# Kernel tuning notes

Hardware: AMD Instinct MI355X
Metric: run time of the kernel (lower is better)

The kernel has to match this reference:

```python
import jax, jax.numpy as jnp
import numpy as np

EPS = 1e-5
NUM_HEADS = 8
POOL_K = 50
POOL_S = 15
DEPTH = 4


def _conv2d(x, w, b, pad_h, pad_w):
    y = jax.lax.conv_general_dilated(
        x, w, window_strides=(1, 1),
        padding=((pad_h, pad_h), (pad_w, pad_w)),
        dimension_numbers=('NCHW', 'OIHW', 'NCHW'))
    return y + b[None, :, None, None]


def _bn_eval(x, g, b):
    # eval-mode BatchNorm2d with running_mean=0, running_var=1
    s = g / jnp.sqrt(1.0 + EPS)
    return x * s[None, :, None, None] + b[None, :, None, None]


def _layernorm(x, g, b):
    m = x.mean(-1, keepdims=True)
    v = ((x - m) ** 2).mean(-1, keepdims=True)
    return (x - m) / jnp.sqrt(v + EPS) * g + b


def _mha(x, wq, bq, wk, bk, wv, bv, wo, bo):
    B, n, d = x.shape
    def split(h):
        return h.reshape(B, n, NUM_HEADS, -1).transpose(0, 2, 1, 3)  # b h n dk
    q = split(x @ wq.T + bq)
    k = split(x @ wk.T + bk)
    v = split(x @ wv.T + bv)
    dk = q.shape[-1]
    scores = jnp.einsum('bhqd,bhkd->bhqk', q, k) / jnp.sqrt(jnp.float32(dk))
    attn = jax.nn.softmax(scores, axis=-1)
    o = jnp.einsum('bhqk,bhkd->bhqd', attn, v).transpose(0, 2, 1, 3).reshape(B, n, d)
    return o @ wo.T + bo


def _encoder(x, p):
    (g1, b1, g2, b2, wq, bq, wk, bk, wv, bv, wo, bo, f1w, f1b, f2w, f2b) = p
    h = _layernorm(x, g1, b1)
    x = x + _mha(h, wq, bq, wk, bk, wv, bv, wo, bo)
    h = _layernorm(x, g2, b2)
    ff = jax.nn.gelu(h @ f1w.T + f1b, approximate=False) @ f2w.T + f2b
    return x + ff


def _forward(x, tw1, tb1, tw2, tb2, tw3, tb3, tw4, tb4, bn1_g, bn1_b, sw, sb,
             bn2_g, bn2_b, ln1_g, ln1_b, ln2_g, ln2_b, wq, bq, wk, bk, wv, bv,
             wo, bo, f1w, f1b, f2w, f2b, ew, eb, bn3_g, bn3_b, cw, cb):
    B, C, T = x.shape
    xi = x[:, None]  # [B,1,C,T]
    h = jnp.concatenate([
        _conv2d(xi, tw1, tb1, 0, 7),
        _conv2d(xi, tw2, tb2, 0, 12),
        _conv2d(xi, tw3, tb3, 0, 25),
        _conv2d(xi, tw4, tb4, 0, 32)], axis=1)          # [B,D,C,T]
    h = _bn_eval(h, bn1_g, bn1_b)
    h = _conv2d(h, sw, sb, 0, 0)                         # [B,D,1,T]
    h = jax.nn.elu(_bn_eval(h, bn2_g, bn2_b))[:, :, 0]   # [B,D,T]

    npos = (T - POOL_K) // POOL_S + 1
    idx = np.arange(npos)[:, None] * POOL_S + np.arange(POOL_K)  # [n,K]
    win = h[:, :, idx]                                   # [B,D,n,K]
    avg = win.mean(-1)                                   # [B,D,n]
    var = win.var(-1, ddof=1)                            # unbiased, like torch
    vlog = jnp.log(jnp.clip(var, 1e-6, 1e6))
    x1 = avg.transpose(0, 2, 1)                          # [B,n,D]
    x2 = vlog.transpose(0, 2, 1)

    for i in range(DEPTH):
        p = (ln1_g[i], ln1_b[i], ln2_g[i], ln2_b[i], wq[i], bq[i], wk[i], bk[i],
             wv[i], bv[i], wo[i], bo[i], f1w[i], f1b[i], f2w[i], f2b[i])
        x1 = _encoder(x1, p)
        x2 = _encoder(x2, p)

    h = jnp.concatenate([x1[:, :, None, :], x2[:, :, None, :]], axis=2)  # [B,n,2,D]
    h = jax.nn.elu(_bn_eval(_conv2d(h, ew, eb, 0, 0), bn3_g, bn3_b))     # [B,n,1,D]
    return h.reshape(B, -1) @ cw.T + cb


def setup_inputs() -> dict:
    B, C, T, D, n, ff, ncls = 16, 64, 1000, 128, 64, 512, 4
    ks = iter(jax.random.split(jax.random.key(0), 48))
    def nrm(shape, s=0.02):
        return jax.random.normal(next(ks), shape, jnp.float32) * s
    inp = {
        'x': jax.random.normal(next(ks), (B, C, T), jnp.float32),
        'tw1': nrm((D // 4, 1, 1, 15)), 'tb1': jnp.zeros(D // 4),
        'tw2': nrm((D // 4, 1, 1, 25)), 'tb2': jnp.zeros(D // 4),
        'tw3': nrm((D // 4, 1, 1, 51)), 'tb3': jnp.zeros(D // 4),
        'tw4': nrm((D // 4, 1, 1, 65)), 'tb4': jnp.zeros(D // 4),
        'bn1_g': jnp.ones(D), 'bn1_b': jnp.zeros(D),
        'sw': nrm((D, D, C, 1)), 'sb': jnp.zeros(D),
        'bn2_g': jnp.ones(D), 'bn2_b': jnp.zeros(D),
        'ln1_g': jnp.ones((DEPTH, D)), 'ln1_b': jnp.zeros((DEPTH, D)),
        'ln2_g': jnp.ones((DEPTH, D)), 'ln2_b': jnp.zeros((DEPTH, D)),
        'wq': nrm((DEPTH, D, D)), 'bq': jnp.zeros((DEPTH, D)),
        'wk': nrm((DEPTH, D, D)), 'bk': jnp.zeros((DEPTH, D)),
        'wv': nrm((DEPTH, D, D)), 'bv': jnp.zeros((DEPTH, D)),
        'wo': nrm((DEPTH, D, D)), 'bo': jnp.zeros((DEPTH, D)),
        'f1w': nrm((DEPTH, ff, D)), 'f1b': jnp.zeros((DEPTH, ff)),
        'f2w': nrm((DEPTH, D, ff)), 'f2b': jnp.zeros((DEPTH, D)),
        'ew': nrm((n, n, 2, 1)), 'eb': jnp.zeros(n),
        'bn3_g': jnp.ones(n), 'bn3_b': jnp.zeros(n),
        'cw': nrm((ncls, D * n)), 'cb': jnp.zeros(ncls),
    }
    return inp


def reference(x, tw1, tb1, tw2, tb2, tw3, tb3, tw4, tb4, bn1_g, bn1_b, sw, sb,
              bn2_g, bn2_b, ln1_g, ln1_b, ln2_g, ln2_b, wq, bq, wk, bk, wv, bv,
              wo, bo, f1w, f1b, f2w, f2b, ew, eb, bn3_g, bn3_b, cw, cb):
    return _forward(x, tw1, tb1, tw2, tb2, tw3, tb3, tw4, tb4, bn1_g, bn1_b,
                    sw, sb, bn2_g, bn2_b, ln1_g, ln1_b, ln2_g, ln2_b, wq, bq,
                    wk, bk, wv, bv, wo, bo, f1w, f1b, f2w, f2b, ew, eb,
                    bn3_g, bn3_b, cw, cb)
```

## Files before the change

### kernel.cpp

```cpp
#include <hip/hip_runtime.h>
#include <math.h>

typedef unsigned short u16;
typedef __attribute__((ext_vector_type(8))) short frag8;
typedef __attribute__((ext_vector_type(4))) float f32x4;

__device__ __forceinline__ float eluf(float v) { return v > 0.f ? v : expm1f(v); }
__device__ __forceinline__ float geluf(float v) {
  return 0.5f * v * (1.f + erff(v * 0.70710678118654752f));
}
__device__ __forceinline__ u16 f2bf(float f) {
  union { float f; unsigned int i; } v; v.f = f;
  return (u16)((v.i + 0x7fffu + ((v.i >> 16) & 1u)) >> 16);
}

#define BN_S 0.99999500003749969f

__global__ void k_tws1(const float* tw1, const float* tw2, const float* tw3, const float* tw4,
                       const float* tb1, const float* tb2, const float* tb3, const float* tb4,
                       const float* bn1g, const float* bn1b,
                       float* tws1, float* c1) {
  int idx = blockIdx.x * 256 + threadIdx.x;
  if (idx < 8320) {
    int i = idx / 65, u = idx - i * 65;
    int g = i >> 5, il = i & 31;
    const float* tws[4] = {tw1, tw2, tw3, tw4};
    const int P[4] = {7, 12, 25, 32};
    int c = u - 32;
    float s1 = bn1g[i] * BN_S;
    float val = 0.f;
    int p = P[g];
    if (c >= -p && c <= p) val = s1 * tws[g][il * (2 * p + 1) + (c + p)];
    tws1[idx] = val;
  } else if (idx < 8448) {
    int i = idx - 8320;
    int g = i >> 5, il = i & 31;
    const float* tbs[4] = {tb1, tb2, tb3, tb4};
    float s1 = bn1g[i] * BN_S;
    c1[i] = s1 * tbs[g][il] + bn1b[i];
  }
}

__global__ __launch_bounds__(256) void k_weff(const float* __restrict__ sw, const float* __restrict__ sb,
                                              const float* __restrict__ tws1, const float* __restrict__ c1,
                                              u16* __restrict__ Wb, float* __restrict__ biasEff) {
  __shared__ float swl[8192];
  __shared__ float tl[8320];
  const int tid = threadIdx.x, lane = tid & 63, wave = tid >> 6;
  const int o = blockIdx.x;
  for (int idx = tid; idx < 8192; idx += 256) swl[idx] = sw[o * 8192 + idx];
  for (int idx = tid; idx < 8320; idx += 256) tl[idx] = tws1[idx];
  __syncthreads();

  #pragma unroll 1
  for (int j = 0; j < 4; j++) {
    int u0 = (wave + 4 * j) * 4;
    float a[4][4];
    #pragma unroll
    for (int uu = 0; uu < 4; uu++)
      #pragma unroll
      for (int r = 0; r < 4; r++) a[uu][r] = 0.f;
    #pragma unroll 1
    for (int i = 0; i < 128; i += 4) {
      #pragma unroll
      for (int ii = 0; ii < 4; ii++) {
        float s = swl[(i + ii) * 64 + lane];
        #pragma unroll
        for (int uu = 0; uu < 4; uu++)
          a[uu][ii] = fmaf(s, tl[(i + ii) * 65 + u0 + uu], a[uu][ii]);
      }
    }
    #pragma unroll
    for (int uu = 0; uu < 4; uu++)
      Wb[((u0 + uu) * 128 + o) * 64 + lane] = f2bf((a[uu][0] + a[uu][1]) + (a[uu][2] + a[uu][3]));
  }

  if (wave == 0) {
    float a[4] = {0.f, 0.f, 0.f, 0.f};
    #pragma unroll 1
    for (int i = 0; i < 128; i += 4) {
      #pragma unroll
      for (int ii = 0; ii < 4; ii++)
        a[ii] = fmaf(swl[(i + ii) * 64 + lane], tl[(i + ii) * 65 + 64], a[ii]);
    }
    Wb[(64 * 128 + o) * 64 + lane] = f2bf((a[0] + a[1]) + (a[2] + a[3]));
  } else if (wave == 1) {
    float pa = 0.f;
    #pragma unroll 8
    for (int i = 0; i < 128; i++)
      pa = fmaf(swl[i * 64 + lane], c1[i], pa);
    #pragma unroll
    for (int off = 32; off; off >>= 1) pa += __shfl_xor(pa, off);
    if (lane == 0) biasEff[o] = pa + sb[o];
  }
}

__global__ __launch_bounds__(256) void k_conv(const float* __restrict__ x,
                                              const u16* __restrict__ Wb,
                                              const float* __restrict__ biasEff,
                                              const float* __restrict__ bn2g, const float* __restrict__ bn2b,
                                              float* __restrict__ z) {
  __shared__ u16 xs[128 * 88];
  const int tid = threadIdx.x;
  const int t0 = blockIdx.x * 64;
  const int o0 = blockIdx.y * 32;
  const int b  = blockIdx.z;

  #pragma unroll
  for (int i = 0; i < 8; i++) {
    int pos = tid + i * 256;
    int kh = pos >> 5;
    int tt = (pos & 31) * 4;
    int gt = t0 - 32 + tt;
    const float* xp = x + (b * 64 + kh) * 1000;
    float v[4];
    if (gt >= 0 && gt + 3 < 1000) {
      float4 f = *(const float4*)(xp + gt);
      v[0] = f.x; v[1] = f.y; v[2] = f.z; v[3] = f.w;
    } else {
      #pragma unroll
      for (int e = 0; e < 4; e++) { int g2 = gt + e; v[e] = (g2 >= 0 && g2 < 1000) ? xp[g2] : 0.f; }
    }
    #pragma unroll
    for (int e = 0; e < 4; e++) xs[(tt + e) * 88 + kh] = f2bf(v[e]);
  }
  __syncthreads();

  const int lane = tid & 63, wave = tid >> 6;
  const int wt = (wave & 1) * 32;
  const int wo = (wave >> 1) * 16;
  const int m = lane & 15, q = lane >> 4;

  f32x4 acc[2];
  #pragma unroll
  for (int i = 0; i < 2; i++) acc[i] = (f32x4){0.f, 0.f, 0.f, 0.f};

  #pragma unroll 2
  for (int u = 0; u < 65; u++) {
    frag8 A[2][2], B[2];
    #pragma unroll
    for (int tp = 0; tp < 2; tp++)
      #pragma unroll
      for (int kc = 0; kc < 2; kc++)
        A[tp][kc] = *(const frag8*)&xs[(wt + tp * 16 + m + u) * 88 + kc * 32 + q * 8];
    #pragma unroll
    for (int kc = 0; kc < 2; kc++)
      B[kc] = *(const frag8*)(Wb + ((u * 128) + o0 + wo + m) * 64 + kc * 32 + q * 8);
    #pragma unroll
    for (int tp = 0; tp < 2; tp++) {
      acc[tp] = __builtin_amdgcn_mfma_f32_16x16x32_bf16(A[tp][0], B[0], acc[tp], 0, 0, 0);
      acc[tp] = __builtin_amdgcn_mfma_f32_16x16x32_bf16(A[tp][1], B[1], acc[tp], 0, 0, 0);
    }
  }

  {
    int o = o0 + wo + m;
    float s2 = bn2g[o] * BN_S;
    float be = biasEff[o], b2 = bn2b[o];
    #pragma unroll
    for (int tp = 0; tp < 2; tp++) {
      #pragma unroll
      for (int r = 0; r < 4; r++) {
        int t = t0 + wt + tp * 16 + q * 4 + r;
        if (t < 1000)
          z[(b * 128 + o) * 1000 + t] = eluf((acc[tp][r] + be) * s2 + b2);
      }
    }
  }
}

__global__ __launch_bounds__(256) void k_pool(const float* __restrict__ z, float* __restrict__ X) {
  __shared__ float zl[16 * 1001];
  int b = blockIdx.x, og = blockIdx.y;
  int tid = threadIdx.x;
  const float* zb = z + (b * 128 + og * 16) * 1000;
  #pragma unroll 1
  for (int r = 0; r < 16; r++)
    for (int c = tid; c < 1000; c += 256) zl[r * 1001 + c] = zb[r * 1000 + c];
  __syncthreads();

  int ol = tid & 15;
  int pb = tid >> 4;
  #pragma unroll 1
  for (int pass = 0; pass < 4; pass++) {
    int p = pb + pass * 16;
    const float* zp = zl + ol * 1001 + p * 15;
    float s = 0.f, ss = 0.f;
    #pragma unroll
    for (int k = 0; k < 50; k++) { float v = zp[k]; s += v; ss = fmaf(v, v, ss); }
    float m = s * 0.02f;
    float var = (ss - s * m) * (1.f / 49.f);
    var = fminf(fmaxf(var, 1e-6f), 1e6f);
    int o = og * 16 + ol;
    X[(b * 64 + p) * 128 + o] = m;
    X[((16 + b) * 64 + p) * 128 + o] = logf(var);
  }
}

__global__ __launch_bounds__(256) void k_cvt6(const float* __restrict__ wq, const float* __restrict__ wk,
                                              const float* __restrict__ wv, const float* __restrict__ wo,
                                              const float* __restrict__ f1w, const float* __restrict__ f2w,
                                              u16* __restrict__ out) {
  int i = blockIdx.x * 256 + threadIdx.x;
  if (i >= 196608) return;
  int fi = i * 4;
  const float* src; int off;
  if      (fi < 65536)  { src = wq;  off = fi; }
  else if (fi < 131072) { src = wk;  off = fi - 65536; }
  else if (fi < 196608) { src = wv;  off = fi - 131072; }
  else if (fi < 262144) { src = wo;  off = fi - 196608; }
  else if (fi < 524288) { src = f1w; off = fi - 262144; }
  else                  { src = f2w; off = fi - 524288; }
  float4 v = *(const float4*)(src + off);
  ushort4 p;
  p.x = f2bf(v.x); p.y = f2bf(v.y); p.z = f2bf(v.z); p.w = f2bf(v.w);
  *(ushort4*)(out + fi) = p;
}

__device__ __forceinline__ void ln128(const float* __restrict__ Xs, u16* __restrict__ Hs,
                                      const float* __restrict__ g, const float* __restrict__ b,
                                      int lane, int wave) {
  float g0 = g[lane], g1 = g[64 + lane], b0 = b[lane], b1 = b[64 + lane];
  #pragma unroll
  for (int rr = 0; rr < 8; rr++) {
    int r = wave * 8 + rr;
    float v0 = Xs[r * 132 + lane], v1 = Xs[r * 132 + 64 + lane];
    float s_ = v0 + v1;
    #pragma unroll
    for (int off = 32; off; off >>= 1) s_ += __shfl_xor(s_, off);
    float mn = s_ * (1.f / 128.f);
    float d0 = v0 - mn, d1 = v1 - mn;
    float qq = d0 * d0 + d1 * d1;
    #pragma unroll
    for (int off = 32; off; off >>= 1) qq += __shfl_xor(qq, off);
    float rs = rsqrtf(qq * (1.f / 128.f) + 1e-5f);
    Hs[r * 136 + lane]      = f2bf(d0 * rs * g0 + b0);
    Hs[r * 136 + 64 + lane] = f2bf(d1 * rs * g1 + b1);
  }
}

__device__ __forceinline__ void gemm_hoist(const frag8 Ar[4][4], const frag8 Bf[4], f32x4 acc[4]) {
  #pragma unroll
  for (int kc = 0; kc < 4; kc++)
    #pragma unroll
    for (int mt = 0; mt < 4; mt++)
      acc[mt] = __builtin_amdgcn_mfma_f32_16x16x32_bf16(Ar[mt][kc], Bf[kc], acc[mt], 0, 0, 0);
}

__device__ __forceinline__ void gemm_pref(const u16* __restrict__ Asrc, int astride,
                                          const frag8 Bf[4], int m, int q, f32x4 acc[4]) {
  #pragma unroll
  for (int kc = 0; kc < 4; kc++) {
    #pragma unroll
    for (int mt = 0; mt < 4; mt++) {
      frag8 Af = *(const frag8*)(Asrc + (mt * 16 + m) * astride + kc * 32 + q * 8);
      acc[mt] = __builtin_amdgcn_mfma_f32_16x16x32_bf16(Af, Bf[kc], acc[mt], 0, 0, 0);
    }
  }
}

__global__ __launch_bounds__(512, 1) void k_enc(float* __restrict__ X,
                                                const u16* __restrict__ Wenc,
                                                const float* __restrict__ ln1g, const float* __restrict__ ln1b,
                                                const float* __restrict__ ln2g, const float* __restrict__ ln2b,
                                                const float* __restrict__ bq, const float* __restrict__ bk,
                                                const float* __restrict__ bv, const float* __restrict__ bo,
                                                const float* __restrict__ f1b, const float* __restrict__ f2b) {
  __shared__ __align__(16) float Xs[64 * 132];
  __shared__ __align__(16) u16   Hs[64 * 136];
  __shared__ __align__(16) u16   Qb[8 * 64 * 32];
  __shared__ __align__(16) u16   Kb[8 * 64 * 32];
  __shared__ __align__(16) u16   VtAO[8 * 16 * 80 + 64 * 136];
  u16* Vt   = VtAO;
  u16* AOs  = VtAO + 10240;
  u16* F1a  = VtAO;
  u16* F1b_ = VtAO + 8704;

  const int tid = threadIdx.x;
  const int lane = tid & 63, wave = tid >> 6;
  const int m = lane & 15, q = lane >> 4;
  const int n0 = wave * 16;
  float* Xg = X + blockIdx.x * 64 * 128;

  const u16* WQ  = Wenc;
  const u16* WK  = Wenc + 65536;
  const u16* WV  = Wenc + 131072;
  const u16* WO  = Wenc + 196608;
  const u16* F1W = Wenc + 262144;
  const u16* F2W = Wenc + 524288;

  u16* Qh = Qb + wave * 2048;
  u16* Kh = Kb + wave * 2048;
  u16* Vh = Vt + wave * 1280;

  for (int i = tid; i < 8192; i += 512) Xs[(i >> 7) * 132 + (i & 127)] = Xg[i];
  __syncthreads();

  #pragma unroll 1
  for (int l = 0; l < 4; l++) {
    const u16* wqb  = WQ  + l * 16384;
    const u16* wkb  = WK  + l * 16384;
    const u16* wvb  = WV  + l * 16384;
    const u16* wob  = WO  + l * 16384;
    const u16* f1wb = F1W + l * 65536;
    const u16* f2wb = F2W + l * 65536;

    frag8 fq[4], fk[4], fv[4];
    #pragma unroll
    for (int kc = 0; kc < 4; kc++) {
      fq[kc] = *(const frag8*)(wqb + (n0 + m) * 128 + kc * 32 + q * 8);
      fk[kc] = *(const frag8*)(wkb + (n0 + m) * 128 + kc * 32 + q * 8);
      fv[kc] = *(const frag8*)(wvb + (n0 + m) * 128 + kc * 32 + q * 8);
    }

    ln128(Xs, Hs, ln1g + l * 128, ln1b + l * 128, lane, wave);
    __syncthreads();

    frag8 fo[4];
    #pragma unroll
    for (int kc = 0; kc < 4; kc++)
      fo[kc] = *(const frag8*)(wob + (n0 + m) * 128 + kc * 32 + q * 8);
    {
      frag8 Ar[4][4];
      #pragma unroll
      for (int mt = 0; mt < 4; mt++)
        #pragma unroll
        for (int kc = 0; kc < 4; kc++)
          Ar[mt][kc] = *(const frag8*)&Hs[(mt * 16 + m) * 136 + kc * 32 + q * 8];
      f32x4 aq[4], ak[4], av[4];
      #pragma unroll
      for (int mt = 0; mt < 4; mt++) { aq[mt] = (f32x4){0,0,0,0}; ak[mt] = (f32x4){0,0,0,0}; av[mt] = (f32x4){0,0,0,0}; }
      gemm_hoist(Ar, fq, aq);
      gemm_hoist(Ar, fk, ak);
      gemm_hoist(Ar, fv, av);
      float bqv = bq[l * 128 + n0 + m];
      float bkv = bk[l * 128 + n0 + m];
      float bvv = bv[l * 128 + n0 + m];
      #pragma unroll
      for (int mt = 0; mt < 4; mt++)
        #pragma unroll
        for (int r = 0; r < 4; r++) {
          int row = mt * 16 + q * 4 + r;
          Qh[row * 32 + m] = f2bf((aq[mt][r] + bqv) * 0.25f);
          Kh[row * 32 + m] = f2bf(ak[mt][r] + bkv);
          Vh[m * 80 + row] = f2bf(av[mt][r] + bvv);
        }
      frag8 z8 = {};
      *(frag8*)&Qh[lane * 32 + 16] = z8;
      *(frag8*)&Qh[lane * 32 + 24] = z8;
      *(frag8*)&Kh[lane * 32 + 16] = z8;
      *(frag8*)&Kh[lane * 32 + 24] = z8;
    }

    frag8 f1f[4];
    #pragma unroll
    for (int kc = 0; kc < 4; kc++)
      f1f[kc] = *(const frag8*)(f1wb + (n0 + m) * 128 + kc * 32 + q * 8);
    {
      f32x4 sacc[4][4];
      frag8 QA[4], KB[4];
      #pragma unroll
      for (int mt = 0; mt < 4; mt++) QA[mt] = *(const frag8*)&Qh[(mt * 16 + m) * 32 + q * 8];
      #pragma unroll
      for (int np = 0; np < 4; np++) KB[np] = *(const frag8*)&Kh[(np * 16 + m) * 32 + q * 8];
      #pragma unroll
      for (int mt = 0; mt < 4; mt++)
        #pragma unroll
        for (int np = 0; np < 4; np++)
          sacc[mt][np] = __builtin_amdgcn_mfma_f32_16x16x32_bf16(QA[mt], KB[np], (f32x4){0,0,0,0}, 0, 0, 0);

      float inv[4][4];
      #pragma unroll
      for (int mt = 0; mt < 4; mt++)
        #pragma unroll
        for (int r = 0; r < 4; r++) {
          float mx = fmaxf(fmaxf(sacc[mt][0][r], sacc[mt][1][r]), fmaxf(sacc[mt][2][r], sacc[mt][3][r]));
          #pragma unroll
          for (int off = 1; off < 16; off <<= 1) mx = fmaxf(mx, __shfl_xor(mx, off));
          #pragma unroll
          for (int np = 0; np < 4; np++) sacc[mt][np][r] = __expf(sacc[mt][np][r] - mx);
          float s_ = ((sacc[mt][0][r] + sacc[mt][1][r]) + (sacc[mt][2][r] + sacc[mt][3][r]));
          #pragma unroll
          for (int off = 1; off < 16; off <<= 1) s_ += __shfl_xor(s_, off);
          inv[mt][r] = 1.f / s_;
        }

      #pragma unroll
      for (int mt = 0; mt < 4; mt++)
        #pragma unroll
        for (int np = 0; np < 4; np++) {
          u16* dst = (np < 2) ? Qh : Kh;
          int col = (np & 1) * 16 + m;
          #pragma unroll
          for (int r = 0; r < 4; r++)
            dst[(mt * 16 + q * 4 + r) * 32 + col] = f2bf(sacc[mt][np][r] * inv[mt][r]);
        }

      f32x4 oacc[4];
      #pragma unroll
      for (int mt = 0; mt < 4; mt++) oacc[mt] = (f32x4){0,0,0,0};
      #pragma unroll
      for (int kc = 0; kc < 2; kc++) {
        frag8 VB = *(const frag8*)&Vh[m * 80 + kc * 32 + q * 8];
        const u16* Psrc = kc ? Kh : Qh;
        #pragma unroll
        for (int mt = 0; mt < 4; mt++) {
          frag8 PA = *(const frag8*)&Psrc[(mt * 16 + m) * 32 + q * 8];
          oacc[mt] = __builtin_amdgcn_mfma_f32_16x16x32_bf16(PA, VB, oacc[mt], 0, 0, 0);
        }
      }
      #pragma unroll
      for (int mt = 0; mt < 4; mt++)
        #pragma unroll
        for (int r = 0; r < 4; r++)
          AOs[(mt * 16 + q * 4 + r) * 136 + wave * 16 + m] = f2bf(oacc[mt][r]);
    }
    __syncthreads();

    {
      f32x4 ao4[4];
      #pragma unroll
      for (int mt = 0; mt < 4; mt++) ao4[mt] = (f32x4){0,0,0,0};
      gemm_pref(AOs, 136, fo, m, q, ao4);
      float bov = bo[l * 128 + n0 + m];
      #pragma unroll
      for (int mt = 0; mt < 4; mt++)
        #pragma unroll
        for (int r = 0; r < 4; r++)
          Xs[(mt * 16 + q * 4 + r) * 132 + n0 + m] += ao4[mt][r] + bov;
    }
    __syncthreads();

    ln128(Xs, Hs, ln2g + l * 128, ln2b + l * 128, lane, wave);
    __syncthreads();

    {
      frag8 Ar[4][4];
      #pragma unroll
      for (int mt = 0; mt < 4; mt++)
        #pragma unroll
        for (int kc = 0; kc < 4; kc++)
          Ar[mt][kc] = *(const frag8*)&Hs[(mt * 16 + m) * 136 + kc * 32 + q * 8];
      f32x4 acc2[4];
      #pragma unroll
      for (int mt = 0; mt < 4; mt++) acc2[mt] = (f32x4){0,0,0,0};
      #pragma unroll 1
      for (int c = 0; c < 4; c++) {
        frag8 f2f[4];
        #pragma unroll
        for (int kc = 0; kc < 4; kc++)
          f2f[kc] = *(const frag8*)(f2wb + (n0 + m) * 512 + c * 128 + kc * 32 + q * 8);
        u16* F1c = (c & 1) ? F1b_ : F1a;
        {
          f32x4 a1[4];
          #pragma unroll
          for (int mt = 0; mt < 4; mt++) a1[mt] = (f32x4){0,0,0,0};
          gemm_hoist(Ar, f1f, a1);
          float b1v = f1b[l * 512 + c * 128 + n0 + m];
          #pragma unroll
          for (int mt = 0; mt < 4; mt++)
            #pragma unroll
            for (int r = 0; r < 4; r++)
              F1c[(mt * 16 + q * 4 + r) * 136 + n0 + m] = f2bf(geluf(a1[mt][r] + b1v));
        }
        __syncthreads();
        if (c < 3) {
          #pragma unroll
          for (int kc = 0; kc < 4; kc++)
            f1f[kc] = *(const frag8*)(f1wb + ((c + 1) * 128 + n0 + m) * 128 + kc * 32 + q * 8);
        }
        gemm_pref(F1c, 136, f2f, m, q, acc2);
      }
      float b2v = f2b[l * 128 + n0 + m];
      #pragma unroll
      for (int mt = 0; mt < 4; mt++)
        #pragma unroll
        for (int r = 0; r < 4; r++)
          Xs[(mt * 16 + q * 4 + r) * 132 + n0 + m] += acc2[mt][r] + b2v;
    }
    __syncthreads();
  }

  for (int i = tid; i < 8192; i += 512) Xg[i] = Xs[(i >> 7) * 132 + (i & 127)];
}

__global__ __launch_bounds__(256) void k_head1(const float* __restrict__ X, const float* __restrict__ ew,
                                               const float* __restrict__ eb, const float* __restrict__ g3,
                                               const float* __restrict__ b3, float* __restrict__ G) {
  __shared__ float Xs[2][8192];
  int b = blockIdx.x, ot = blockIdx.y;
  int tid = threadIdx.x;
  {
    const float4* x1 = (const float4*)(X + b * 8192);
    const float4* x2 = (const float4*)(X + (16 + b) * 8192);
    float4* s1 = (float4*)&Xs[0][0];
    float4* s2 = (float4*)&Xs[1][0];
    for (int i = tid; i < 2048; i += 256) { s1[i] = x1[i]; s2[i] = x2[i]; }
  }
  __syncthreads();
  int w = tid & 127, og = tid >> 7;
  int oc0 = ot * 16 + og * 8;
  float a[8] = {};
  for (int ic = 0; ic < 64; ic++) {
    float x1v = Xs[0][ic * 128 + w], x2v = Xs[1][ic * 128 + w];
    #pragma unroll
    for (int j = 0; j < 8; j++) {
      a[j] = fmaf(ew[((oc0 + j) * 64 + ic) * 2 + 0], x1v, a[j]);
      a[j] = fmaf(ew[((oc0 + j) * 64 + ic) * 2 + 1], x2v, a[j]);
    }
  }
  #pragma unroll
  for (int j = 0; j < 8; j++) {
    int oc = oc0 + j;
    float v = (a[j] + eb[oc]) * (g3[oc] * BN_S) + b3[oc];
    G[(b * 64 + oc) * 128 + w] = eluf(v);
  }
}

__global__ __launch_bounds__(256) void k_head2(const float* __restrict__ G, const float* __restrict__ cw,
                                               const float* __restrict__ cb, float* __restrict__ out) {
  __shared__ float red[256];
  int b = blockIdx.x, c = blockIdx.y, tid = threadIdx.x;
  const float4* g4 = (const float4*)(G + b * 8192);
  const float4* c4 = (const float4*)(cw + c * 8192);
  float p = 0.f;
  for (int i = tid; i < 2048; i += 256) {
    float4 g = g4[i], w = c4[i];
    p += g.x * w.x + g.y * w.y + g.z * w.z + g.w * w.w;
  }
  red[tid] = p;
  __syncthreads();
  for (int s = 128; s > 0; s >>= 1) {
    if (tid < s) red[tid] += red[tid + s];
    __syncthreads();
  }
  if (tid == 0) out[b * 4 + c] = red[0] + cb[c];
}

extern "C" void kernel_launch(void* const* d_in, const int* in_sizes, int n_in,
                              void* d_out, int out_size, void* d_ws, size_t ws_size,
                              hipStream_t stream) {
  const float* x    = (const float*)d_in[0];
  const float* tw1  = (const float*)d_in[1];  const float* tb1 = (const float*)d_in[2];
  const float* tw2  = (const float*)d_in[3];  const float* tb2 = (const float*)d_in[4];
  const float* tw3  = (const float*)d_in[5];  const float* tb3 = (const float*)d_in[6];
  const float* tw4  = (const float*)d_in[7];  const float* tb4 = (const float*)d_in[8];
  const float* bn1g = (const float*)d_in[9];  const float* bn1b = (const float*)d_in[10];
  const float* sw   = (const float*)d_in[11]; const float* sb   = (const float*)d_in[12];
  const float* bn2g = (const float*)d_in[13]; const float* bn2b = (const float*)d_in[14];
  const float* ln1g = (const float*)d_in[15]; const float* ln1b = (const float*)d_in[16];
  const float* ln2g = (const float*)d_in[17]; const float* ln2b = (const float*)d_in[18];
  const float* wq   = (const float*)d_in[19]; const float* bq   = (const float*)d_in[20];
  const float* wk   = (const float*)d_in[21]; const float* bk   = (const float*)d_in[22];
  const float* wv   = (const float*)d_in[23]; const float* bv   = (const float*)d_in[24];
  const float* wo   = (const float*)d_in[25]; const float* bo   = (const float*)d_in[26];
  const float* f1w  = (const float*)d_in[27]; const float* f1b  = (const float*)d_in[28];
  const float* f2w  = (const float*)d_in[29]; const float* f2b  = (const float*)d_in[30];
  const float* ew   = (const float*)d_in[31]; const float* eb   = (const float*)d_in[32];
  const float* g3   = (const float*)d_in[33]; const float* b3   = (const float*)d_in[34];
  const float* cw   = (const float*)d_in[35]; const float* cb   = (const float*)d_in[36];

  float* ws      = (float*)d_ws;
  float* tws1    = ws;
  float* c1      = ws + 8320;
  float* biasEff = ws + 8448;
  u16*   Wb      = (u16*)(ws + 8576);
  float* z       = ws + 541056;
  float* X       = ws + 2589056;
  u16*   Wenc    = (u16*)(ws + 3113344);
  float* G       = z;

  k_cvt6<<<768, 256, 0, stream>>>(wq, wk, wv, wo, f1w, f2w, Wenc);
  k_tws1<<<33, 256, 0, stream>>>(tw1, tw2, tw3, tw4, tb1, tb2, tb3, tb4, bn1g, bn1b, tws1, c1);
  k_weff<<<128, 256, 0, stream>>>(sw, sb, tws1, c1, Wb, biasEff);
  k_conv<<<dim3(16, 4, 16), 256, 0, stream>>>(x, Wb, biasEff, bn2g, bn2b, z);
  k_pool<<<dim3(16, 8), 256, 0, stream>>>(z, X);

  k_enc<<<32, 512, 0, stream>>>(X, Wenc, ln1g, ln1b, ln2g, ln2b, bq, bk, bv, bo, f1b, f2b);

  k_head1<<<dim3(16, 4), 256, 0, stream>>>(X, ew, eb, g3, b3, G);
  k_head2<<<dim3(16, 4), 256, 0, stream>>>(G, cw, cb, (float*)d_out);
}
```

Measured before the change: 384.2 us.

## Fuse prep kernels and head kernels, widen conv tile, restructure encoder FFN buffering

Merges the weight-conversion and temporal-weight prep kernels into k_weff, and merges the two head kernels into one per-batch kernel that keeps G in shared memory. This cuts the launch count from eight to five. The conv kernel now computes 64 output channels per block with a register-prefetched B fragment, so each LDS-staged x tile is reused more. The encoder FFN writes all four GELU chunks into a shared pool before running the second GEMM with prefetched weights, which removes the per-chunk barriers. The cost is fewer conv blocks and lower parallelism in the head and conv grids, plus higher LDS use in the encoder.

Result: slower. 403.0 us (+4.9%).

```diff
diff --git a/kernel.cpp b/kernel.cpp
--- a/kernel.cpp
+++ b/kernel.cpp
@@ -16,40 +16,59 @@
 
 #define BN_S 0.99999500003749969f
 
-__global__ void k_tws1(const float* tw1, const float* tw2, const float* tw3, const float* tw4,
-                       const float* tb1, const float* tb2, const float* tb3, const float* tb4,
-                       const float* bn1g, const float* bn1b,
-                       float* tws1, float* c1) {
-  int idx = blockIdx.x * 256 + threadIdx.x;
-  if (idx < 8320) {
-    int i = idx / 65, u = idx - i * 65;
-    int g = i >> 5, il = i & 31;
-    const float* tws[4] = {tw1, tw2, tw3, tw4};
-    const int P[4] = {7, 12, 25, 32};
-    int c = u - 32;
-    float s1 = bn1g[i] * BN_S;
-    float val = 0.f;
-    int p = P[g];
-    if (c >= -p && c <= p) val = s1 * tws[g][il * (2 * p + 1) + (c + p)];
-    tws1[idx] = val;
-  } else if (idx < 8448) {
-    int i = idx - 8320;
-    int g = i >> 5, il = i & 31;
-    const float* tbs[4] = {tb1, tb2, tb3, tb4};
-    float s1 = bn1g[i] * BN_S;
-    c1[i] = s1 * tbs[g][il] + bn1b[i];
-  }
-}
-
-__global__ __launch_bounds__(256) void k_weff(const float* __restrict__ sw, const float* __restrict__ sb,
-                                              const float* __restrict__ tws1, const float* __restrict__ c1,
-                                              u16* __restrict__ Wb, float* __restrict__ biasEff) {
+__global__ __launch_bounds__(256) void k_weff(const float* __restrict__ tw1, const float* __restrict__ tw2,
+                                              const float* __restrict__ tw3, const float* __restrict__ tw4,
+                                              const float* __restrict__ tb1, const float* __restrict__ tb2,
+                                              const float* __restrict__ tb3, const float* __restrict__ tb4,
+                                              const float* __restrict__ bn1g, const float* __restrict__ bn1b,
+                                              const float* __restrict__ sw, const float* __restrict__ sb,
+                                              const float* __restrict__ wq, const float* __restrict__ wk,
+                                              const float* __restrict__ wv, const float* __restrict__ wo,
+                                              const float* __restrict__ f1w, const float* __restrict__ f2w,
+                                              u16* __restrict__ Wb, float* __restrict__ biasEff,
+                                              u16* __restrict__ Wenc) {
   __shared__ float swl[8192];
   __shared__ float tl[8320];
+  __shared__ float c1l[128];
   const int tid = threadIdx.x, lane = tid & 63, wave = tid >> 6;
   const int o = blockIdx.x;
+
   for (int idx = tid; idx < 8192; idx += 256) swl[idx] = sw[o * 8192 + idx];
-  for (int idx = tid; idx < 8320; idx += 256) tl[idx] = tws1[idx];
+  {
+    const float* tws4[4] = {tw1, tw2, tw3, tw4};
+    const int P[4] = {7, 12, 25, 32};
+    for (int idx = tid; idx < 8320; idx += 256) {
+      int i = idx / 65, u = idx - i * 65;
+      int g = i >> 5, il = i & 31;
+      int c = u - 32;
+      float s1 = bn1g[i] * BN_S;
+      float val = 0.f;
+      int p = P[g];
+      if (c >= -p && c <= p) val = s1 * tws4[g][il * (2 * p + 1) + (c + p)];
+      tl[idx] = val;
+    }
+    const float* tbs[4] = {tb1, tb2, tb3, tb4};
+    for (int i = tid; i < 128; i += 256) {
+      int g = i >> 5, il = i & 31;
+      float s1 = bn1g[i] * BN_S;
+      c1l[i] = s1 * tbs[g][il] + bn1b[i];
+    }
+  }
+
+  for (int i = blockIdx.x * 256 + tid; i < 196608; i += 128 * 256) {
+    int fi = i * 4;
+    const float* src; int off;
+    if      (fi < 65536)  { src = wq;  off = fi; }
+    else if (fi < 131072) { src = wk;  off = fi - 65536; }
+    else if (fi < 196608) { src = wv;  off = fi - 131072; }
+    else if (fi < 262144) { src = wo;  off = fi - 196608; }
+    else if (fi < 524288) { src = f1w; off = fi - 262144; }
+    else                  { src = f2w; off = fi - 524288; }
+    float4 v = *(const float4*)(src + off);
+    ushort4 p;
+    p.x = f2bf(v.x); p.y = f2bf(v.y); p.z = f2bf(v.z); p.w = f2bf(v.w);
+    *(ushort4*)(Wenc + fi) = p;
+  }
   __syncthreads();
 
   #pragma unroll 1
@@ -88,7 +107,7 @@
     float pa = 0.f;
     #pragma unroll 8
     for (int i = 0; i < 128; i++)
-      pa = fmaf(swl[i * 64 + lane], c1[i], pa);
+      pa = fmaf(swl[i * 64 + lane], c1l[i], pa);
     #pragma unroll
     for (int off = 32; off; off >>= 1) pa += __shfl_xor(pa, off);
     if (lane == 0) biasEff[o] = pa + sb[o];
@@ -103,7 +122,7 @@
   __shared__ u16 xs[128 * 88];
   const int tid = threadIdx.x;
   const int t0 = blockIdx.x * 64;
-  const int o0 = blockIdx.y * 32;
+  const int o0 = blockIdx.y * 64;
   const int b  = blockIdx.z;
 
   #pragma unroll
@@ -128,33 +147,54 @@
 
   const int lane = tid & 63, wave = tid >> 6;
   const int wt = (wave & 1) * 32;
-  const int wo = (wave >> 1) * 16;
+  const int wo = (wave >> 1) * 32;
   const int m = lane & 15, q = lane >> 4;
 
-  f32x4 acc[2];
+  f32x4 acc[2][2];
   #pragma unroll
-  for (int i = 0; i < 2; i++) acc[i] = (f32x4){0.f, 0.f, 0.f, 0.f};
-
-  #pragma unroll 2
+  for (int i = 0; i < 2; i++)
+    #pragma unroll
+    for (int j = 0; j < 2; j++) acc[i][j] = (f32x4){0.f, 0.f, 0.f, 0.f};
+
+  frag8 Bc[2][2];
+  #pragma unroll
+  for (int op = 0; op < 2; op++)
+    #pragma unroll
+    for (int kc = 0; kc < 2; kc++)
+      Bc[op][kc] = *(const frag8*)(Wb + (o0 + wo + op * 16 + m) * 64 + kc * 32 + q * 8);
+
+  #pragma unroll 1
   for (int u = 0; u < 65; u++) {
-    frag8 A[2][2], B[2];
+    frag8 Bn[2][2];
+    int un = (u < 64) ? u + 1 : 64;
+    #pragma unroll
+    for (int op = 0; op < 2; op++)
+      #pragma unroll
+      for (int kc = 0; kc < 2; kc++)
+        Bn[op][kc] = *(const frag8*)(Wb + ((un * 128) + o0 + wo + op * 16 + m) * 64 + kc * 32 + q * 8);
+    frag8 A[2][2];
     #pragma unroll
     for (int tp = 0; tp < 2; tp++)
       #pragma unroll
       for (int kc = 0; kc < 2; kc++)
         A[tp][kc] = *(const frag8*)&xs[(wt + tp * 16 + m + u) * 88 + kc * 32 + q * 8];
     #pragma unroll
-    for (int kc = 0; kc < 2; kc++)
-      B[kc] = *(const frag8*)(Wb + ((u * 128) + o0 + wo + m) * 64 + kc * 32 + q * 8);
-    #pragma unroll
-    for (int tp = 0; tp < 2; tp++) {
-      acc[tp] = __builtin_amdgcn_mfma_f32_16x16x32_bf16(A[tp][0], B[0], acc[tp], 0, 0, 0);
-      acc[tp] = __builtin_amdgcn_mfma_f32_16x16x32_bf16(A[tp][1], B[1], acc[tp], 0, 0, 0);
-    }
-  }
-
-  {
-    int o = o0 + wo + m;
+    for (int tp = 0; tp < 2; tp++)
+      #pragma unroll
+      for (int op = 0; op < 2; op++) {
+        acc[tp][op] = __builtin_amdgcn_mfma_f32_16x16x32_bf16(A[tp][0], Bc[op][0], acc[tp][op], 0, 0, 0);
+        acc[tp][op] = __builtin_amdgcn_mfma_f32_16x16x32_bf16(A[tp][1], Bc[op][1], acc[tp][op], 0, 0, 0);
+      }
+    #pragma unroll
+    for (int op = 0; op < 2; op++)
+      #pragma unroll
+      for (int kc = 0; kc < 2; kc++)
+        Bc[op][kc] = Bn[op][kc];
+  }
+
+  #pragma unroll
+  for (int op = 0; op < 2; op++) {
+    int o = o0 + wo + op * 16 + m;
     float s2 = bn2g[o] * BN_S;
     float be = biasEff[o], b2 = bn2b[o];
     #pragma unroll
@@ -163,7 +203,7 @@
       for (int r = 0; r < 4; r++) {
         int t = t0 + wt + tp * 16 + q * 4 + r;
         if (t < 1000)
-          z[(b * 128 + o) * 1000 + t] = eluf((acc[tp][r] + be) * s2 + b2);
+          z[(b * 128 + o) * 1000 + t] = eluf((acc[tp][op][r] + be) * s2 + b2);
       }
     }
   }
@@ -197,26 +237,6 @@
   }
 }
 
-__global__ __launch_bounds__(256) void k_cvt6(const float* __restrict__ wq, const float* __restrict__ wk,
-                                              const float* __restrict__ wv, const float* __restrict__ wo,
-                                              const float* __restrict__ f1w, const float* __restrict__ f2w,
-                                              u16* __restrict__ out) {
-  int i = blockIdx.x * 256 + threadIdx.x;
-  if (i >= 196608) return;
-  int fi = i * 4;
-  const float* src; int off;
-  if      (fi < 65536)  { src = wq;  off = fi; }
-  else if (fi < 131072) { src = wk;  off = fi - 65536; }
-  else if (fi < 196608) { src = wv;  off = fi - 131072; }
-  else if (fi < 262144) { src = wo;  off = fi - 196608; }
-  else if (fi < 524288) { src = f1w; off = fi - 262144; }
-  else                  { src = f2w; off = fi - 524288; }
-  float4 v = *(const float4*)(src + off);
-  ushort4 p;
-  p.x = f2bf(v.x); p.y = f2bf(v.y); p.z = f2bf(v.z); p.w = f2bf(v.w);
-  *(ushort4*)(out + fi) = p;
-}
-
 __device__ __forceinline__ void ln128(const float* __restrict__ Xs, u16* __restrict__ Hs,
                                       const float* __restrict__ g, const float* __restrict__ b,
                                       int lane, int wave) {
@@ -268,13 +288,8 @@
                                                 const float* __restrict__ f1b, const float* __restrict__ f2b) {
   __shared__ __align__(16) float Xs[64 * 132];
   __shared__ __align__(16) u16   Hs[64 * 136];
-  __shared__ __align__(16) u16   Qb[8 * 64 * 32];
-  __shared__ __align__(16) u16   Kb[8 * 64 * 32];
-  __shared__ __align__(16) u16   VtAO[8 * 16 * 80 + 64 * 136];
-  u16* Vt   = VtAO;
-  u16* AOs  = VtAO + 10240;
-  u16* F1a  = VtAO;
-  u16* F1b_ = VtAO + 8704;
+  __shared__ __align__(16) u16   Pool[43008];
+  u16* AOs = Hs;
 
   const int tid = threadIdx.x;
   const int lane = tid & 63, wave = tid >> 6;
@@ -289,9 +304,9 @@
   const u16* F1W = Wenc + 262144;
   const u16* F2W = Wenc + 524288;
 
-  u16* Qh = Qb + wave * 2048;
-  u16* Kh = Kb + wave * 2048;
-  u16* Vh = Vt + wave * 1280;
+  u16* Qh = Pool + wave * 2048;
+  u16* Kh = Pool + 16384 + wave * 2048;
+  u16* Vh = Pool + 32768 + wave * 1280;
 
   for (int i = tid; i < 8192; i += 512) Xs[(i >> 7) * 132 + (i & 127)] = Xg[i];
   __syncthreads();
@@ -441,35 +456,49 @@
         #pragma unroll
         for (int kc = 0; kc < 4; kc++)
           Ar[mt][kc] = *(const frag8*)&Hs[(mt * 16 + m) * 136 + kc * 32 + q * 8];
-      f32x4 acc2[4];
-      #pragma unroll
-      for (int mt = 0; mt < 4; mt++) acc2[mt] = (f32x4){0,0,0,0};
       #pragma unroll 1
       for (int c = 0; c < 4; c++) {
-        frag8 f2f[4];
-        #pragma unroll
-        for (int kc = 0; kc < 4; kc++)
-          f2f[kc] = *(const frag8*)(f2wb + (n0 + m) * 512 + c * 128 + kc * 32 + q * 8);
-        u16* F1c = (c & 1) ? F1b_ : F1a;
-        {
-          f32x4 a1[4];
-          #pragma unroll
-          for (int mt = 0; mt < 4; mt++) a1[mt] = (f32x4){0,0,0,0};
-          gemm_hoist(Ar, f1f, a1);
-          float b1v = f1b[l * 512 + c * 128 + n0 + m];
-          #pragma unroll
-          for (int mt = 0; mt < 4; mt++)
-            #pragma unroll
-            for (int r = 0; r < 4; r++)
-              F1c[(mt * 16 + q * 4 + r) * 136 + n0 + m] = f2bf(geluf(a1[mt][r] + b1v));
-        }
-        __syncthreads();
+        f32x4 a1[4];
+        #pragma unroll
+        for (int mt = 0; mt < 4; mt++) a1[mt] = (f32x4){0,0,0,0};
+        gemm_hoist(Ar, f1f, a1);
         if (c < 3) {
           #pragma unroll
           for (int kc = 0; kc < 4; kc++)
             f1f[kc] = *(const frag8*)(f1wb + ((c + 1) * 128 + n0 + m) * 128 + kc * 32 + q * 8);
         }
-        gemm_pref(F1c, 136, f2f, m, q, acc2);
+        float b1v = f1b[l * 512 + c * 128 + n0 + m];
+        u16* F1c = Pool + c * 8704;
+        #pragma unroll
+        for (int mt = 0; mt < 4; mt++)
+          #pragma unroll
+          for (int r = 0; r < 4; r++)
+            F1c[(mt * 16 + q * 4 + r) * 136 + n0 + m] = f2bf(geluf(a1[mt][r] + b1v));
+      }
+    }
+    __syncthreads();
+
+    {
+      f32x4 acc2[4];
+      #pragma unroll
+      for (int mt = 0; mt < 4; mt++) acc2[mt] = (f32x4){0,0,0,0};
+      frag8 f2f[4];
+      #pragma unroll
+      for (int kc = 0; kc < 4; kc++)
+        f2f[kc] = *(const frag8*)(f2wb + (n0 + m) * 512 + kc * 32 + q * 8);
+      #pragma unroll 1
+      for (int c = 0; c < 4; c++) {
+        frag8 f2n[4];
+        if (c < 3) {
+          #pragma unroll
+          for (int kc = 0; kc < 4; kc++)
+            f2n[kc] = *(const frag8*)(f2wb + (n0 + m) * 512 + (c + 1) * 128 + kc * 32 + q * 8);
+        }
+        gemm_pref(Pool + c * 8704, 136, f2f, m, q, acc2);
+        if (c < 3) {
+          #pragma unroll
+          for (int kc = 0; kc < 4; kc++) f2f[kc] = f2n[kc];
+        }
       }
       float b2v = f2b[l * 128 + n0 + m];
       #pragma unroll
@@ -484,11 +513,14 @@
   for (int i = tid; i < 8192; i += 512) Xg[i] = Xs[(i >> 7) * 132 + (i & 127)];
 }
 
-__global__ __launch_bounds__(256) void k_head1(const float* __restrict__ X, const float* __restrict__ ew,
-                                               const float* __restrict__ eb, const float* __restrict__ g3,
-                                               const float* __restrict__ b3, float* __restrict__ G) {
+__global__ __launch_bounds__(256) void k_head(const float* __restrict__ X, const float* __restrict__ ew,
+                                              const float* __restrict__ eb, const float* __restrict__ g3,
+                                              const float* __restrict__ b3, const float* __restrict__ cw,
+                                              const float* __restrict__ cb, float* __restrict__ out) {
   __shared__ float Xs[2][8192];
-  int b = blockIdx.x, ot = blockIdx.y;
+  __shared__ float Gs[8192];
+  __shared__ float red[256];
+  int b = blockIdx.x;
   int tid = threadIdx.x;
   {
     const float4* x1 = (const float4*)(X + b * 8192);
@@ -499,42 +531,44 @@
   }
   __syncthreads();
   int w = tid & 127, og = tid >> 7;
-  int oc0 = ot * 16 + og * 8;
-  float a[8] = {};
-  for (int ic = 0; ic < 64; ic++) {
-    float x1v = Xs[0][ic * 128 + w], x2v = Xs[1][ic * 128 + w];
+  #pragma unroll 1
+  for (int ot = 0; ot < 4; ot++) {
+    int oc0 = ot * 16 + og * 8;
+    float a[8] = {};
+    for (int ic = 0; ic < 64; ic++) {
+      float x1v = Xs[0][ic * 128 + w], x2v = Xs[1][ic * 128 + w];
+      #pragma unroll
+      for (int j = 0; j < 8; j++) {
+        a[j] = fmaf(ew[((oc0 + j) * 64 + ic) * 2 + 0], x1v, a[j]);
+        a[j] = fmaf(ew[((oc0 + j) * 64 + ic) * 2 + 1], x2v, a[j]);
+      }
+    }
     #pragma unroll
     for (int j = 0; j < 8; j++) {
-      a[j] = fmaf(ew[((oc0 + j) * 64 + ic) * 2 + 0], x1v, a[j]);
-      a[j] = fmaf(ew[((oc0 + j) * 64 + ic) * 2 + 1], x2v, a[j]);
-    }
-  }
-  #pragma unroll
-  for (int j = 0; j < 8; j++) {
-    int oc = oc0 + j;
-    float v = (a[j] + eb[oc]) * (g3[oc] * BN_S) + b3[oc];
-    G[(b * 64 + oc) * 128 + w] = eluf(v);
-  }
-}
-
-__global__ __launch_bounds__(256) void k_head2(const float* __restrict__ G, const float* __restrict__ cw,
-                                               const float* __restrict__ cb, float* __restrict__ out) {
-  __shared__ float red[256];
-  int b = blockIdx.x, c = blockIdx.y, tid = threadIdx.x;
-  const float4* g4 = (const float4*)(G + b * 8192);
-  const float4* c4 = (const float4*)(cw + c * 8192);
-  float p = 0.f;
-  for (int i = tid; i < 2048; i += 256) {
-    float4 g = g4[i], w = c4[i];
-    p += g.x * w.x + g.y * w.y + g.z * w.z + g.w * w.w;
-  }
-  red[tid] = p;
+      int oc = oc0 + j;
+      float v = (a[j] + eb[oc]) * (g3[oc] * BN_S) + b3[oc];
+      Gs[oc * 128 + w] = eluf(v);
+    }
+  }
   __syncthreads();
-  for (int s = 128; s > 0; s >>= 1) {
-    if (tid < s) red[tid] += red[tid + s];
-    __syncthreads();
-  }
-  if (tid == 0) out[b * 4 + c] = red[0] + cb[c];
+  #pragma unroll 1
+  for (int c = 0; c < 4; c++) {
+    const float4* g4 = (const float4*)Gs;
+    const float4* c4 = (const float4*)(cw + c * 8192);
+    float p = 0.f;
+    for (int i = tid; i < 2048; i += 256) {
+      float4 g = g4[i], wv = c4[i];
+      p += g.x * wv.x + g.y * wv.y + g.z * wv.z + g.w * wv.w;
+    }
+    red[tid] = p;
+    __syncthreads();
+    for (int s = 128; s > 0; s >>= 1) {
+      if (tid < s) red[tid] += red[tid + s];
+      __syncthreads();
+    }
+    if (tid == 0) out[b * 4 + c] = red[0] + cb[c];
+    __syncthreads();
+  }
 }
 
 extern "C" void kernel_launch(void* const* d_in, const int* in_sizes, int n_in,
@@ -561,23 +595,16 @@
   const float* cw   = (const float*)d_in[35]; const float* cb   = (const float*)d_in[36];
 
   float* ws      = (float*)d_ws;
-  float* tws1    = ws;
-  float* c1      = ws + 8320;
   float* biasEff = ws + 8448;
   u16*   Wb      = (u16*)(ws + 8576);
   float* z       = ws + 541056;
   float* X       = ws + 2589056;
   u16*   Wenc    = (u16*)(ws + 3113344);
-  float* G       = z;
-
-  k_cvt6<<<768, 256, 0, stream>>>(wq, wk, wv, wo, f1w, f2w, Wenc);
-  k_tws1<<<33, 256, 0, stream>>>(tw1, tw2, tw3, tw4, tb1, tb2, tb3, tb4, bn1g, bn1b, tws1, c1);
-  k_weff<<<128, 256, 0, stream>>>(sw, sb, tws1, c1, Wb, biasEff);
-  k_conv<<<dim3(16, 4, 16), 256, 0, stream>>>(x, Wb, biasEff, bn2g, bn2b, z);
+
+  k_weff<<<128, 256, 0, stream>>>(tw1, tw2, tw3, tw4, tb1, tb2, tb3, tb4, bn1g, bn1b,
+                                  sw, sb, wq, wk, wv, wo, f1w, f2w, Wb, biasEff, Wenc);
+  k_conv<<<dim3(16, 2, 16), 256, 0, stream>>>(x, Wb, biasEff, bn2g, bn2b, z);
   k_pool<<<dim3(16, 8), 256, 0, stream>>>(z, X);
-
   k_enc<<<32, 512, 0, stream>>>(X, Wenc, ln1g, ln1b, ln2g, ln2b, bq, bk, bv, bo, f1b, f2b);
-
-  k_head1<<<dim3(16, 4), 256, 0, stream>>>(X, ew, eb, g3, b3, G);
-  k_head2<<<dim3(16, 4), 256, 0, stream>>>(G, cw, cb, (float*)d_out);
-}
+  k_head<<<16, 256, 0, stream>>>(X, ew, eb, g3, b3, cw, cb, (float*)d_out);
+}
```

## Reparallelize weight fusion and pooling, widen conv tile, batch encoder FFN stages

Applied to the files above, without the earlier changes.

k_weff now runs one output element per wave over a 66x32 grid and reads global memory directly, replacing 128 blocks that each staged large shared arrays. k_conv gives each wave 32 output channels, which halves the number of blocks and lets each block reuse its staged input tile for more MFMAs. k_pool uses one thread per (position, channel) with no shared staging, which spreads the work over many more blocks. In the encoder FFN, all four GELU chunks are written to a shared pool before a single barrier, followed by the second GEMM with prefetched weights. This removes the per-chunk barriers but needs more shared memory per block.

Result: faster. 351.2 us (-8.6%).

```diff
diff --git a/kernel.cpp b/kernel.cpp
--- a/kernel.cpp
+++ b/kernel.cpp
@@ -44,51 +44,26 @@
 __global__ __launch_bounds__(256) void k_weff(const float* __restrict__ sw, const float* __restrict__ sb,
                                               const float* __restrict__ tws1, const float* __restrict__ c1,
                                               u16* __restrict__ Wb, float* __restrict__ biasEff) {
-  __shared__ float swl[8192];
-  __shared__ float tl[8320];
-  const int tid = threadIdx.x, lane = tid & 63, wave = tid >> 6;
-  const int o = blockIdx.x;
-  for (int idx = tid; idx < 8192; idx += 256) swl[idx] = sw[o * 8192 + idx];
-  for (int idx = tid; idx < 8320; idx += 256) tl[idx] = tws1[idx];
-  __syncthreads();
-
-  #pragma unroll 1
-  for (int j = 0; j < 4; j++) {
-    int u0 = (wave + 4 * j) * 4;
-    float a[4][4];
-    #pragma unroll
-    for (int uu = 0; uu < 4; uu++)
-      #pragma unroll
-      for (int r = 0; r < 4; r++) a[uu][r] = 0.f;
-    #pragma unroll 1
+  const int lane = threadIdx.x & 63, wave = threadIdx.x >> 6;
+  const int u = blockIdx.x;
+  const int o = blockIdx.y * 4 + wave;
+  const float* swp = sw + o * 8192 + lane;
+  if (u < 65) {
+    const float* tp = tws1 + u;
+    float a0 = 0.f, a1 = 0.f, a2 = 0.f, a3 = 0.f;
+    #pragma unroll 8
     for (int i = 0; i < 128; i += 4) {
-      #pragma unroll
-      for (int ii = 0; ii < 4; ii++) {
-        float s = swl[(i + ii) * 64 + lane];
-        #pragma unroll
-        for (int uu = 0; uu < 4; uu++)
-          a[uu][ii] = fmaf(s, tl[(i + ii) * 65 + u0 + uu], a[uu][ii]);
-      }
-    }
-    #pragma unroll
-    for (int uu = 0; uu < 4; uu++)
-      Wb[((u0 + uu) * 128 + o) * 64 + lane] = f2bf((a[uu][0] + a[uu][1]) + (a[uu][2] + a[uu][3]));
-  }
-
-  if (wave == 0) {
-    float a[4] = {0.f, 0.f, 0.f, 0.f};
-    #pragma unroll 1
-    for (int i = 0; i < 128; i += 4) {
-      #pragma unroll
-      for (int ii = 0; ii < 4; ii++)
-        a[ii] = fmaf(swl[(i + ii) * 64 + lane], tl[(i + ii) * 65 + 64], a[ii]);
-    }
-    Wb[(64 * 128 + o) * 64 + lane] = f2bf((a[0] + a[1]) + (a[2] + a[3]));
-  } else if (wave == 1) {
+      a0 = fmaf(swp[(i + 0) * 64], tp[(i + 0) * 65], a0);
+      a1 = fmaf(swp[(i + 1) * 64], tp[(i + 1) * 65], a1);
+      a2 = fmaf(swp[(i + 2) * 64], tp[(i + 2) * 65], a2);
+      a3 = fmaf(swp[(i + 3) * 64], tp[(i + 3) * 65], a3);
+    }
+    Wb[(u * 128 + o) * 64 + lane] = f2bf((a0 + a1) + (a2 + a3));
+  } else {
     float pa = 0.f;
     #pragma unroll 8
     for (int i = 0; i < 128; i++)
-      pa = fmaf(swl[i * 64 + lane], c1[i], pa);
+      pa = fmaf(swp[i * 64], c1[i], pa);
     #pragma unroll
     for (int off = 32; off; off >>= 1) pa += __shfl_xor(pa, off);
     if (lane == 0) biasEff[o] = pa + sb[o];
@@ -103,7 +78,7 @@
   __shared__ u16 xs[128 * 88];
   const int tid = threadIdx.x;
   const int t0 = blockIdx.x * 64;
-  const int o0 = blockIdx.y * 32;
+  const int o0 = blockIdx.y * 64;
   const int b  = blockIdx.z;
 
   #pragma unroll
@@ -128,33 +103,40 @@
 
   const int lane = tid & 63, wave = tid >> 6;
   const int wt = (wave & 1) * 32;
-  const int wo = (wave >> 1) * 16;
+  const int wo = (wave >> 1) * 32;
   const int m = lane & 15, q = lane >> 4;
 
-  f32x4 acc[2];
-  #pragma unroll
-  for (int i = 0; i < 2; i++) acc[i] = (f32x4){0.f, 0.f, 0.f, 0.f};
+  f32x4 acc[2][2];
+  #pragma unroll
+  for (int i = 0; i < 2; i++)
+    #pragma unroll
+    for (int j = 0; j < 2; j++) acc[i][j] = (f32x4){0.f, 0.f, 0.f, 0.f};
 
   #pragma unroll 2
   for (int u = 0; u < 65; u++) {
-    frag8 A[2][2], B[2];
+    frag8 A[2][2], B[2][2];
     #pragma unroll
     for (int tp = 0; tp < 2; tp++)
       #pragma unroll
       for (int kc = 0; kc < 2; kc++)
         A[tp][kc] = *(const frag8*)&xs[(wt + tp * 16 + m + u) * 88 + kc * 32 + q * 8];
     #pragma unroll
-    for (int kc = 0; kc < 2; kc++)
-      B[kc] = *(const frag8*)(Wb + ((u * 128) + o0 + wo + m) * 64 + kc * 32 + q * 8);
-    #pragma unroll
-    for (int tp = 0; tp < 2; tp++) {
-      acc[tp] = __builtin_amdgcn_mfma_f32_16x16x32_bf16(A[tp][0], B[0], acc[tp], 0, 0, 0);
-      acc[tp] = __builtin_amdgcn_mfma_f32_16x16x32_bf16(A[tp][1], B[1], acc[tp], 0, 0, 0);
-    }
-  }
-
-  {
-    int o = o0 + wo + m;
+    for (int op = 0; op < 2; op++)
+      #pragma unroll
+      for (int kc = 0; kc < 2; kc++)
+        B[op][kc] = *(const frag8*)(Wb + ((u * 128) + o0 + wo + op * 16 + m) * 64 + kc * 32 + q * 8);
+    #pragma unroll
+    for (int tp = 0; tp < 2; tp++)
+      #pragma unroll
+      for (int op = 0; op < 2; op++) {
+        acc[tp][op] = __builtin_amdgcn_mfma_f32_16x16x32_bf16(A[tp][0], B[op][0], acc[tp][op], 0, 0, 0);
+        acc[tp][op] = __builtin_amdgcn_mfma_f32_16x16x32_bf16(A[tp][1], B[op][1], acc[tp][op], 0, 0, 0);
+      }
+  }
+
+  #pragma unroll
+  for (int op = 0; op < 2; op++) {
+    int o = o0 + wo + op * 16 + m;
     float s2 = bn2g[o] * BN_S;
     float be = biasEff[o], b2 = bn2b[o];
     #pragma unroll
@@ -163,38 +145,23 @@
       for (int r = 0; r < 4; r++) {
         int t = t0 + wt + tp * 16 + q * 4 + r;
         if (t < 1000)
-          z[(b * 128 + o) * 1000 + t] = eluf((acc[tp][r] + be) * s2 + b2);
+          z[(b * 128 + o) * 1000 + t] = eluf((acc[tp][op][r] + be) * s2 + b2);
       }
     }
   }
 }
 
-__global__ __launch_bounds__(256) void k_pool(const float* __restrict__ z, float* __restrict__ X) {
-  __shared__ float zl[16 * 1001];
-  int b = blockIdx.x, og = blockIdx.y;
-  int tid = threadIdx.x;
-  const float* zb = z + (b * 128 + og * 16) * 1000;
-  #pragma unroll 1
-  for (int r = 0; r < 16; r++)
-    for (int c = tid; c < 1000; c += 256) zl[r * 1001 + c] = zb[r * 1000 + c];
-  __syncthreads();
-
-  int ol = tid & 15;
-  int pb = tid >> 4;
-  #pragma unroll 1
-  for (int pass = 0; pass < 4; pass++) {
-    int p = pb + pass * 16;
-    const float* zp = zl + ol * 1001 + p * 15;
-    float s = 0.f, ss = 0.f;
-    #pragma unroll
-    for (int k = 0; k < 50; k++) { float v = zp[k]; s += v; ss = fmaf(v, v, ss); }
-    float m = s * 0.02f;
-    float var = (ss - s * m) * (1.f / 49.f);
-    var = fminf(fmaxf(var, 1e-6f), 1e6f);
-    int o = og * 16 + ol;
-    X[(b * 64 + p) * 128 + o] = m;
-    X[((16 + b) * 64 + p) * 128 + o] = logf(var);
-  }
+__global__ __launch_bounds__(128) void k_pool(const float* __restrict__ z, float* __restrict__ X) {
+  int p = blockIdx.x, b = blockIdx.y, o = threadIdx.x;
+  const float* zp = z + (b * 128 + o) * 1000 + p * 15;
+  float s = 0.f, ss = 0.f;
+  #pragma unroll
+  for (int k = 0; k < 50; k++) { float v = zp[k]; s += v; ss = fmaf(v, v, ss); }
+  float m = s * 0.02f;
+  float var = (ss - s * m) * (1.f / 49.f);
+  var = fminf(fmaxf(var, 1e-6f), 1e6f);
+  X[(b * 64 + p) * 128 + o] = m;
+  X[((16 + b) * 64 + p) * 128 + o] = logf(var);
 }
 
 __global__ __launch_bounds__(256) void k_cvt6(const float* __restrict__ wq, const float* __restrict__ wk,
@@ -268,13 +235,8 @@
                                                 const float* __restrict__ f1b, const float* __restrict__ f2b) {
   __shared__ __align__(16) float Xs[64 * 132];
   __shared__ __align__(16) u16   Hs[64 * 136];
-  __shared__ __align__(16) u16   Qb[8 * 64 * 32];
-  __shared__ __align__(16) u16   Kb[8 * 64 * 32];
-  __shared__ __align__(16) u16   VtAO[8 * 16 * 80 + 64 * 136];
-  u16* Vt   = VtAO;
-  u16* AOs  = VtAO + 10240;
-  u16* F1a  = VtAO;
-  u16* F1b_ = VtAO + 8704;
+  __shared__ __align__(16) u16   Pool[43008];
+  u16* AOs = Hs;
 
   const int tid = threadIdx.x;
   const int lane = tid & 63, wave = tid >> 6;
@@ -289,9 +251,9 @@
   const u16* F1W = Wenc + 262144;
   const u16* F2W = Wenc + 524288;
 
-  u16* Qh = Qb + wave * 2048;
-  u16* Kh = Kb + wave * 2048;
-  u16* Vh = Vt + wave * 1280;
+  u16* Qh = Pool + wave * 2048;
+  u16* Kh = Pool + 16384 + wave * 2048;
+  u16* Vh = Pool + 32768 + wave * 1280;
 
   for (int i = tid; i < 8192; i += 512) Xs[(i >> 7) * 132 + (i & 127)] = Xg[i];
   __syncthreads();
@@ -441,35 +403,49 @@
         #pragma unroll
         for (int kc = 0; kc < 4; kc++)
           Ar[mt][kc] = *(const frag8*)&Hs[(mt * 16 + m) * 136 + kc * 32 + q * 8];
-      f32x4 acc2[4];
-      #pragma unroll
-      for (int mt = 0; mt < 4; mt++) acc2[mt] = (f32x4){0,0,0,0};
       #pragma unroll 1
       for (int c = 0; c < 4; c++) {
-        frag8 f2f[4];
-        #pragma unroll
-        for (int kc = 0; kc < 4; kc++)
-          f2f[kc] = *(const frag8*)(f2wb + (n0 + m) * 512 + c * 128 + kc * 32 + q * 8);
-        u16* F1c = (c & 1) ? F1b_ : F1a;
-        {
-          f32x4 a1[4];
-          #pragma unroll
-          for (int mt = 0; mt < 4; mt++) a1[mt] = (f32x4){0,0,0,0};
-          gemm_hoist(Ar, f1f, a1);
-          float b1v = f1b[l * 512 + c * 128 + n0 + m];
-          #pragma unroll
-          for (int mt = 0; mt < 4; mt++)
-            #pragma unroll
-            for (int r = 0; r < 4; r++)
-              F1c[(mt * 16 + q * 4 + r) * 136 + n0 + m] = f2bf(geluf(a1[mt][r] + b1v));
-        }
-        __syncthreads();
+        f32x4 a1[4];
+        #pragma unroll
+        for (int mt = 0; mt < 4; mt++) a1[mt] = (f32x4){0,0,0,0};
+        gemm_hoist(Ar, f1f, a1);
         if (c < 3) {
           #pragma unroll
           for (int kc = 0; kc < 4; kc++)
             f1f[kc] = *(const frag8*)(f1wb + ((c + 1) * 128 + n0 + m) * 128 + kc * 32 + q * 8);
         }
-        gemm_pref(F1c, 136, f2f, m, q, acc2);
+        float b1v = f1b[l * 512 + c * 128 + n0 + m];
+        u16* F1c = Pool + c * 8704;
+        #pragma unroll
+        for (int mt = 0; mt < 4; mt++)
+          #pragma unroll
+          for (int r = 0; r < 4; r++)
+            F1c[(mt * 16 + q * 4 + r) * 136 + n0 + m] = f2bf(geluf(a1[mt][r] + b1v));
+      }
+    }
+    __syncthreads();
+
+    {
+      f32x4 acc2[4];
+      #pragma unroll
+      for (int mt = 0; mt < 4; mt++) acc2[mt] = (f32x4){0,0,0,0};
+      frag8 f2f[4];
+      #pragma unroll
+      for (int kc = 0; kc < 4; kc++)
+        f2f[kc] = *(const frag8*)(f2wb + (n0 + m) * 512 + kc * 32 + q * 8);
+      #pragma unroll 1
+      for (int c = 0; c < 4; c++) {
+        frag8 f2n[4];
+        if (c < 3) {
+          #pragma unroll
+          for (int kc = 0; kc < 4; kc++)
+            f2n[kc] = *(const frag8*)(f2wb + (n0 + m) * 512 + (c + 1) * 128 + kc * 32 + q * 8);
+        }
+        gemm_pref(Pool + c * 8704, 136, f2f, m, q, acc2);
+        if (c < 3) {
+          #pragma unroll
+          for (int kc = 0; kc < 4; kc++) f2f[kc] = f2n[kc];
+        }
       }
       float b2v = f2b[l * 128 + n0 + m];
       #pragma unroll
@@ -572,9 +548,9 @@
 
   k_cvt6<<<768, 256, 0, stream>>>(wq, wk, wv, wo, f1w, f2w, Wenc);
   k_tws1<<<33, 256, 0, stream>>>(tw1, tw2, tw3, tw4, tb1, tb2, tb3, tb4, bn1g, bn1b, tws1, c1);
-  k_weff<<<128, 256, 0, stream>>>(sw, sb, tws1, c1, Wb, biasEff);
-  k_conv<<<dim3(16, 4, 16), 256, 0, stream>>>(x, Wb, biasEff, bn2g, bn2b, z);
-  k_pool<<<dim3(16, 8), 256, 0, stream>>>(z, X);
+  k_weff<<<dim3(66, 32), 256, 0, stream>>>(sw, sb, tws1, c1, Wb, biasEff);
+  k_conv<<<dim3(16, 2, 16), 256, 0, stream>>>(x, Wb, biasEff, bn2g, bn2b, z);
+  k_pool<<<dim3(64, 16), 128, 0, stream>>>(z, X);
 
   k_enc<<<32, 512, 0, stream>>>(X, Wenc, ln1g, ln1b, ln2g, ln2b, bq, bk, bv, bo, f1b, f2b);
 
```
